# Kernel optimization log

Hardware: AMD Instinct MI355X
Metric: run time of the kernel (lower is better)

Reference implementation:

```python
import jax, jax.numpy as jnp
import numpy as np

BIG = 1e9
EPS_BETA = 1e-6
EPS_BN = 1e-5

N_NODES = 50000
N_EDGES = 800000
IN_DIM = 128
OUT_DIM = 128


def setup_inputs() -> dict:
    key = jax.random.key(0)
    ks = jax.random.split(key, 8)
    h = jax.random.normal(ks[0], (N_NODES, IN_DIM), dtype=jnp.float32)
    src = jax.random.randint(ks[1], (N_EDGES,), 0, N_NODES, dtype=jnp.int32)
    dst = jax.random.randint(ks[2], (N_EDGES,), 0, N_NODES, dtype=jnp.int32)
    sigma_GD = jax.random.uniform(ks[3], (N_EDGES,), dtype=jnp.float32)
    fc_w = jax.random.normal(ks[4], (IN_DIM, OUT_DIM), dtype=jnp.float32) / np.sqrt(IN_DIM)
    fc_b = jax.random.normal(ks[5], (OUT_DIM,), dtype=jnp.float32) * 0.01
    attn_w = jax.random.normal(ks[6], (2 * OUT_DIM, 1), dtype=jnp.float32) / np.sqrt(2 * OUT_DIM)
    attn_b = jax.random.normal(ks[7], (1,), dtype=jnp.float32) * 0.01
    bn_gamma = jnp.ones((OUT_DIM,), dtype=jnp.float32)
    bn_beta = jnp.zeros((OUT_DIM,), dtype=jnp.float32)
    return {"h": h, "src": src, "dst": dst, "sigma_GD": sigma_GD,
            "fc_w": fc_w, "fc_b": fc_b, "attn_w": attn_w, "attn_b": attn_b,
            "bn_gamma": bn_gamma, "bn_beta": bn_beta}


def reference(h, src, dst, sigma_GD, fc_w, fc_b, attn_w, attn_b, bn_gamma, bn_beta):
    n = h.shape[0]
    # node projection
    z = h @ fc_w + fc_b                                   # [N, D]
    z = jnp.where(jnp.isinf(z), BIG, z)
    # per-edge attention logits: concat(src,dst) @ W == src@W1 + dst@W2 (avoid concat materialization)
    d = z.shape[1]
    w_src, w_dst = attn_w[:d], attn_w[d:]
    z_src = z[src]                                        # [E, D]
    a = z_src @ w_src + z[dst] @ w_dst + attn_b           # [E, 1]
    a = jnp.where(jnp.isinf(a), BIG, a)
    e = jax.nn.leaky_relu(a, negative_slope=0.01)[:, 0]   # [E]
    # segment softmax over incoming edges (mailbox softmax)
    m = jax.ops.segment_max(e, dst, num_segments=n)       # [N]
    ex = jnp.exp(e - m[dst])
    denom = jax.ops.segment_sum(ex, dst, num_segments=n)  # [N]
    alpha = ex / denom[dst]                               # [E]
    # beta: sigma_GD normalized per destination node
    bsum = jax.ops.segment_sum(sigma_GD, dst, num_segments=n)
    beta = sigma_GD / (bsum[dst] + EPS_BETA)              # [E]
    # weighted scatter-sum of source features
    h_new = jax.ops.segment_sum((alpha * beta)[:, None] * z_src, dst, num_segments=n)  # [N, D]
    h_new = jnp.where(jnp.isinf(h_new), BIG, h_new)
    # BatchNorm1d (training-mode batch stats, biased variance, as torch does)
    mu = h_new.mean(axis=0)
    var = ((h_new - mu) ** 2).mean(axis=0)
    h_bn = (h_new - mu) * jax.lax.rsqrt(var + EPS_BN) * bn_gamma + bn_beta
    return jax.nn.elu(h_bn)
```

## Files before the change

### kernel.cpp

```cpp
#include <hip/hip_runtime.h>
#include <hip/hip_fp16.h>
#include <math.h>

#define N_NODES 50000
#define N_EDGES 800000
#define BIGV 1000000000.0f
#define NBLK_GEMM 3125
#define CHUNK 1024
#define NCHUNK 782
#define NBUCKET 782
#define NB4 784
#define NHALF 1564
#define BMAX 768
#define OVFSTRIDE 1024

typedef _Float16 half8 __attribute__((ext_vector_type(8)));
typedef float floatx4 __attribute__((ext_vector_type(4)));

__device__ __forceinline__ float clampinf(float x) { return isinf(x) ? BIGV : x; }

__device__ __forceinline__ void barrier_lgkm_only() {
    __builtin_amdgcn_sched_barrier(0);
    asm volatile("s_waitcnt lgkmcnt(0)" ::: "memory");
    __builtin_amdgcn_s_barrier();
    __builtin_amdgcn_sched_barrier(0);
}

__global__ __launch_bounds__(256) void k_prep(const float* __restrict__ W,
                                              __half* __restrict__ wt,
                                              float* __restrict__ bns,
                                              const int* __restrict__ dst,
                                              int* __restrict__ countsT)
{
    __shared__ int hist[NB4];
    const int t = threadIdx.x;
    const int idx = blockIdx.x * 256 + t;
    if (idx < 16384) {
        int n = idx >> 7, k = idx & 127;
        wt[idx] = __float2half(W[k * 128 + n]);
    }
    if (idx < 256) bns[idx] = 0.f;
    for (int i = t; i < NB4; i += 256) hist[i] = 0;
    __syncthreads();
    const int base = blockIdx.x * CHUNK;
    for (int i = t; i < CHUNK; i += 256) {
        int e = base + i;
        if (e < N_EDGES) atomicAdd(&hist[dst[e] >> 6], 1);
    }
    __syncthreads();
    for (int i = t; i < NB4; i += 256)
        countsT[i * NB4 + blockIdx.x] = hist[i];
}

__global__ __launch_bounds__(256) void k_off(const int* __restrict__ countsT,
                                             int* __restrict__ cursC,
                                             int* __restrict__ btot)
{
    const int wv = (blockIdx.x << 2) + (threadIdx.x >> 6);
    const int l = threadIdx.x & 63;
    if (wv >= NBUCKET) {
        if (l == 0 && wv < NB4) btot[wv] = 0;
        return;
    }
    const int* row = countsT + (size_t)wv * NB4;
    int carry = 0;
    #pragma unroll
    for (int p = 0; p < 13; ++p) {
        const int c = p * 64 + l;
        const int v = (c < NCHUNK) ? row[c] : 0;
        int x = v;
        #pragma unroll
        for (int o = 1; o < 64; o <<= 1) {
            int u = __shfl_up(x, o);
            if (l >= o) x += u;
        }
        if (c < NCHUNK) cursC[(size_t)c * NB4 + wv] = carry + x - v;
        carry += __shfl(x, 63);
    }
    if (l == 0) btot[wv] = carry;
}

__global__ __launch_bounds__(256) void k_gemm(
    const float* __restrict__ h, const __half* __restrict__ wt,
    const float* __restrict__ bias, const float* __restrict__ attn_w,
    __half* __restrict__ zh, float* __restrict__ sv, float* __restrict__ tv)
{
    __shared__ _Float16 hA[16][136];
    __shared__ float spart[4][16], tpart[4][16];

    const int tid = threadIdx.x;
    const int lane = tid & 63;
    const int wv = tid >> 6;
    const int l16 = lane & 15;
    const int oct = lane >> 4;
    const int n0 = wv << 5;
    const int node0 = blockIdx.x << 4;

    {
        const float4* h4 = (const float4*)(h + (size_t)node0 * 128);
        for (int i = tid; i < 512; i += 256) {
            int r = i >> 5, c4 = i & 31;
            float4 v = h4[i];
            union { __half2 h2[2]; uint2 u; } pk;
            pk.h2[0] = __floats2half2_rn(v.x, v.y);
            pk.h2[1] = __floats2half2_rn(v.z, v.w);
            *(uint2*)&hA[r][c4 << 2] = pk.u;
        }
    }

    half8 bfrag[4][2];
    #pragma unroll
    for (int kk = 0; kk < 4; ++kk)
        #pragma unroll
        for (int t = 0; t < 2; ++t)
            bfrag[kk][t] = *(const half8*)(wt + (size_t)(n0 + t * 16 + l16) * 128
                                              + kk * 32 + oct * 8);

    const float bv0 = bias[n0 + l16],         bv1 = bias[n0 + 16 + l16];
    const float ws0 = attn_w[n0 + l16],       ws1 = attn_w[n0 + 16 + l16];
    const float wd0 = attn_w[128 + n0 + l16], wd1 = attn_w[128 + n0 + 16 + l16];

    barrier_lgkm_only();

    floatx4 acc0 = {0.f, 0.f, 0.f, 0.f};
    floatx4 acc1 = {0.f, 0.f, 0.f, 0.f};
    #pragma unroll
    for (int kk = 0; kk < 4; ++kk) {
        half8 a = *(const half8*)&hA[l16][(kk << 5) + (oct << 3)];
        acc0 = __builtin_amdgcn_mfma_f32_16x16x32_f16(a, bfrag[kk][0], acc0, 0, 0, 0);
        acc1 = __builtin_amdgcn_mfma_f32_16x16x32_f16(a, bfrag[kk][1], acc1, 0, 0, 0);
    }

    float s_acc[4], t_acc[4];
    #pragma unroll
    for (int r = 0; r < 4; ++r) {
        float z0 = clampinf(acc0[r] + bv0);
        float z1 = clampinf(acc1[r] + bv1);
        const int row = (oct << 2) + r;
        zh[(size_t)(node0 + row) * 128 + n0 + l16]      = __float2half(z0);
        zh[(size_t)(node0 + row) * 128 + n0 + 16 + l16] = __float2half(z1);
        s_acc[r] = z0 * ws0 + z1 * ws1;
        t_acc[r] = z0 * wd0 + z1 * wd1;
    }
    #pragma unroll
    for (int r = 0; r < 4; ++r) {
        #pragma unroll
        for (int o = 1; o < 16; o <<= 1) {
            s_acc[r] += __shfl_xor(s_acc[r], o);
            t_acc[r] += __shfl_xor(t_acc[r], o);
        }
    }
    if (l16 == 0) {
        #pragma unroll
        for (int r = 0; r < 4; ++r) {
            spart[wv][(oct << 2) + r] = s_acc[r];
            tpart[wv][(oct << 2) + r] = t_acc[r];
        }
    }
    barrier_lgkm_only();
    if (tid < 16) {
        sv[node0 + tid] = spart[0][tid] + spart[1][tid] + spart[2][tid] + spart[3][tid];
        tv[node0 + tid] = tpart[0][tid] + tpart[1][tid] + tpart[2][tid] + tpart[3][tid];
    }
}

__global__ __launch_bounds__(256) void k_scat(
    const int* __restrict__ src, const int* __restrict__ dst,
    const float* __restrict__ sigma,
    const float* __restrict__ sv, const float* __restrict__ tv,
    const float* __restrict__ attn_b,
    const int* __restrict__ cursC, const int* __restrict__ btot,
    float4* __restrict__ tmp, int* __restrict__ bbase_g)
{
    __shared__ int cur[NB4];
    __shared__ int bb[NB4];
    __shared__ int tsc[256];
    const int t = threadIdx.x;
    const int self = blockIdx.x;

    for (int i = t; i < NB4; i += 256) cur[i] = cursC[(size_t)self * NB4 + i];

    uint4 bt = {0u, 0u, 0u, 0u};
    int tsum = 0;
    if (t < 196) {
        bt = ((const uint4*)btot)[t];
        tsum = (int)(bt.x + bt.y + bt.z + bt.w);
    }
    tsc[t] = tsum;
    __syncthreads();
    for (int off = 1; off < 256; off <<= 1) {
        int u = (t >= off) ? tsc[t - off] : 0;
        __syncthreads();
        tsc[t] += u;
        __syncthreads();
    }
    if (t < 196) {
        const int v0 = tsc[t] - tsum;
        bb[4*t+0] = v0;
        bb[4*t+1] = v0 + (int)bt.x;
        bb[4*t+2] = v0 + (int)bt.x + (int)bt.y;
        bb[4*t+3] = v0 + (int)bt.x + (int)bt.y + (int)bt.z;
    }
    __syncthreads();
    for (int i = t; i < NB4; i += 256) cur[i] += bb[i];
    if (self == 0)
        for (int i = t; i < NB4; i += 256) bbase_g[i] = bb[i];
    __syncthreads();

    const float ab = attn_b[0];
    const int base = self * CHUNK;
    for (int i = t; i < CHUNK; i += 256) {
        int e = base + i;
        if (e < N_EDGES) {
            int s = src[e];
            int d = dst[e];
            float a = sv[s] + tv[d] + ab;
            a = clampinf(a);
            float ev = a > 0.f ? a : 0.01f * a;
            int pos = atomicAdd(&cur[d >> 6], 1);
            float4 rec;
            rec.x = __int_as_float(s);
            rec.y = sigma[e];
            rec.z = ev;
            rec.w = __int_as_float(d);
            tmp[pos] = rec;
        }
    }
}

__global__ __launch_bounds__(512) void k_bagg(
    const float4* __restrict__ tmp, const int* __restrict__ bbase_g,
    const __half* __restrict__ zh, float4* __restrict__ ovf,
    float* __restrict__ out, float* __restrict__ partials)
{
    __shared__ float4 lrec[BMAX];
    __shared__ int hist[32];
    __shared__ int segs[33];
    __shared__ int cur[32];
    __shared__ float bnS[128], bnQ[128];
    const int t = threadIdx.x;
    const int b2 = blockIdx.x;
    const int b  = b2 >> 1;
    const int hf = b2 & 1;
    const int s0 = bbase_g[b];
    const int n  = bbase_g[b + 1] - s0;

    if (t < 32) hist[t] = 0;
    if (t < 128) { bnS[t] = 0.f; bnQ[t] = 0.f; }
    __syncthreads();
    const float* tw = (const float*)tmp;
    for (int i = t; i < n; i += 512) {
        int d = __float_as_int(tw[4 * (size_t)(s0 + i) + 3]);
        if (((d >> 5) & 1) == hf) atomicAdd(&hist[d & 31], 1);
    }
    __syncthreads();
    if (t < 32) {
        const int hv = hist[t];
        int x = hv;
        #pragma unroll
        for (int o = 1; o < 32; o <<= 1) {
            int u = __shfl_up(x, o);
            if (t >= o) x += u;
        }
        segs[t] = x - hv;
        cur[t]  = x - hv;
        if (t == 31) segs[32] = x;
    }
    __syncthreads();
    for (int i = t; i < n; i += 512) {
        float4 rec = tmp[s0 + i];
        int d = __float_as_int(rec.w);
        if (((d >> 5) & 1) == hf) {
            int pos = atomicAdd(&cur[d & 31], 1);
            if (pos < BMAX) lrec[pos] = rec;
            else            ovf[(size_t)b2 * OVFSTRIDE + (pos - BMAX)] = rec;
        }
    }
    __syncthreads();

    const int lane = t & 63;
    const int wv = t >> 6;
    const int grp = lane >> 4;
    const int l16 = lane & 15;
    float pS[8] = {0.f,0.f,0.f,0.f,0.f,0.f,0.f,0.f};
    float pQ[8] = {0.f,0.f,0.f,0.f,0.f,0.f,0.f,0.f};

    for (int j = wv; j < 32; j += 8) {
        const int node = (b << 6) + (hf << 5) + j;
        if (node >= N_NODES) continue;
        const int beg = segs[j];
        const int deg = segs[j + 1] - beg;
        float acc[8] = {0.f,0.f,0.f,0.f,0.f,0.f,0.f,0.f};

        if (deg > 0) {
            if (deg <= 64) {
                int sidx = 0; float sig = 0.f, e = -INFINITY;
                if (lane < deg) {
                    const int off = beg + lane;
                    float4 r = (off < BMAX) ? lrec[off]
                             : ovf[(size_t)b2 * OVFSTRIDE + (off - BMAX)];
                    sidx = __float_as_int(r.x); sig = r.y; e = r.z;
                }
                float m = e;
                for (int o = 32; o; o >>= 1) m = fmaxf(m, __shfl_xor(m, o));
                float p = (lane < deg) ? __expf(e - m) : 0.f;
                float dn = p, bs = sig;
                for (int o = 32; o; o >>= 1) {
                    dn += __shfl_xor(dn, o);
                    bs += __shfl_xor(bs, o);
                }
                const float coef = p * sig * (1.0f / dn) / (bs + 1e-6f);
                for (int c = 0; c < deg; c += 8) {
                    const int j0 = c + grp, j1 = c + 4 + grp;
                    const int js0 = (j0 < deg) ? j0 : 0;
                    const int js1 = (j1 < deg) ? j1 : 0;
                    float cf0 = __shfl(coef, js0); int sj0 = __shfl(sidx, js0);
                    float cf1 = __shfl(coef, js1); int sj1 = __shfl(sidx, js1);
                    uint4 raw0, raw1;
                    if (j0 < deg)
                        raw0 = *(const uint4*)(zh + ((size_t)sj0 << 7) + (l16 << 3));
                    if (j1 < deg)
                        raw1 = *(const uint4*)(zh + ((size_t)sj1 << 7) + (l16 << 3));
                    if (j0 < deg) {
                        const __half2* hp = (const __half2*)&raw0;
                        #pragma unroll
                        for (int k = 0; k < 4; ++k) {
                            float2 f = __half22float2(hp[k]);
                            acc[2*k]   = fmaf(cf0, f.x, acc[2*k]);
                            acc[2*k+1] = fmaf(cf0, f.y, acc[2*k+1]);
                        }
                    }
                    if (j1 < deg) {
                        const __half2* hp = (const __half2*)&raw1;
                        #pragma unroll
                        for (int k = 0; k < 4; ++k) {
                            float2 f = __half22float2(hp[k]);
                            acc[2*k]   = fmaf(cf1, f.x, acc[2*k]);
                            acc[2*k+1] = fmaf(cf1, f.y, acc[2*k+1]);
                        }
                    }
                }
            } else {
                float m = -INFINITY;
                for (int i = lane; i < deg; i += 64) {
                    const int off = beg + i;
                    float4 r = (off < BMAX) ? lrec[off]
                             : ovf[(size_t)b2 * OVFSTRIDE + (off - BMAX)];
                    m = fmaxf(m, r.z);
                }
                for (int o = 32; o; o >>= 1) m = fmaxf(m, __shfl_xor(m, o));
                float dn = 0.f, bs = 0.f;
                for (int i = lane; i < deg; i += 64) {
                    const int off = beg + i;
                    float4 r = (off < BMAX) ? lrec[off]
                             : ovf[(size_t)b2 * OVFSTRIDE + (off - BMAX)];
                    dn += __expf(r.z - m); bs += r.y;
                }
                for (int o = 32; o; o >>= 1) {
                    dn += __shfl_xor(dn, o);
                    bs += __shfl_xor(bs, o);
                }
                const float scale = (1.0f / dn) / (bs + 1e-6f);
                for (int c = 0; c < deg; c += 64) {
                    int i = c + lane;
                    int sidx = 0; float coef = 0.f;
                    if (i < deg) {
                        const int off = beg + i;
                        float4 r = (off < BMAX) ? lrec[off]
                                 : ovf[(size_t)b2 * OVFSTRIDE + (off - BMAX)];
                        sidx = __float_as_int(r.x);
                        coef = __expf(r.z - m) * r.y * scale;
                    }
                    const int cnt2 = min(64, deg - c);
                    for (int jj = 0; jj < cnt2; jj += 4) {
                        const int j4 = jj + grp;
                        const int js = (j4 < cnt2) ? j4 : 0;
                        float cf = __shfl(coef, js);
                        int sj = __shfl(sidx, js);
                        if (j4 < cnt2) {
                            uint4 raw = *(const uint4*)(zh + ((size_t)sj << 7) + (l16 << 3));
                            const __half2* hp = (const __half2*)&raw;
                            #pragma unroll
                            for (int k = 0; k < 4; ++k) {
                                float2 f = __half22float2(hp[k]);
                                acc[2*k]   = fmaf(cf, f.x, acc[2*k]);
                                acc[2*k+1] = fmaf(cf, f.y, acc[2*k+1]);
                            }
                        }
                    }
                }
            }
        }
        #pragma unroll
        for (int k = 0; k < 8; ++k) {
            acc[k] += __shfl_xor(acc[k], 16);
            acc[k] += __shfl_xor(acc[k], 32);
        }
        if (grp == 0) {
            float o[8];
            #pragma unroll
            for (int k = 0; k < 8; ++k) {
                o[k] = clampinf(acc[k]);
                pS[k] += o[k];
                pQ[k] += o[k] * o[k];
            }
            float4 o0, o1;
            o0.x = o[0]; o0.y = o[1]; o0.z = o[2]; o0.w = o[3];
            o1.x = o[4]; o1.y = o[5]; o1.z = o[6]; o1.w = o[7];
            float4* op = (float4*)(out + (size_t)node * 128 + (l16 << 3));
            op[0] = o0; op[1] = o1;
        }
    }
    if (grp == 0) {
        #pragma unroll
        for (int k = 0; k < 8; ++k) {
            atomicAdd(&bnS[(l16 << 3) + k], pS[k]);
            atomicAdd(&bnQ[(l16 << 3) + k], pQ[k]);
        }
    }
    __syncthreads();
    if (t < 128) {
        partials[(size_t)b2 * 256 + t]       = bnS[t];
        partials[(size_t)b2 * 256 + 128 + t] = bnQ[t];
    }
}

__global__ __launch_bounds__(256) void k_bnred(const float* __restrict__ partials,
                                               float* __restrict__ bns)
{
    const int t = threadIdx.x;
    const int r0 = blockIdx.x * 25;
    const int r1 = min(r0 + 25, NHALF);
    float s = 0.f;
    for (int r = r0; r < r1; ++r) s += partials[(size_t)r * 256 + t];
    atomicAdd(&bns[t], s);
}

__global__ __launch_bounds__(256) void k_bnapply(float* __restrict__ io,
                                                 const float* __restrict__ sums,
                                                 const float* __restrict__ gamma,
                                                 const float* __restrict__ beta)
{
    __shared__ float sc[128], sh[128];
    const int tid = threadIdx.x;
    if (tid < 128) {
        const float invn = 1.0f / (float)N_NODES;
        float mu = sums[tid] * invn;
        float var = fmaxf(sums[128 + tid] * invn - mu * mu, 0.f);
        float g = gamma[tid] * rsqrtf(var + 1e-5f);
        sc[tid] = g;
        sh[tid] = beta[tid] - mu * g;
    }
    __syncthreads();
    const size_t idx = (size_t)blockIdx.x * 256 + tid;
    const int f4 = ((int)idx & 31) << 2;
    float4 x = ((const float4*)io)[idx];
    float y0 = x.x * sc[f4 + 0] + sh[f4 + 0];
    float y1 = x.y * sc[f4 + 1] + sh[f4 + 1];
    float y2 = x.z * sc[f4 + 2] + sh[f4 + 2];
    float y3 = x.w * sc[f4 + 3] + sh[f4 + 3];
    float4 o;
    o.x = y0 > 0.f ? y0 : expm1f(y0);
    o.y = y1 > 0.f ? y1 : expm1f(y1);
    o.z = y2 > 0.f ? y2 : expm1f(y2);
    o.w = y3 > 0.f ? y3 : expm1f(y3);
    ((float4*)io)[idx] = o;
}

extern "C" void kernel_launch(void* const* d_in, const int* in_sizes, int n_in,
                              void* d_out, int out_size, void* d_ws, size_t ws_size,
                              hipStream_t stream)
{
    const float* h      = (const float*)d_in[0];
    const int*   src    = (const int*)  d_in[1];
    const int*   dst    = (const int*)  d_in[2];
    const float* sigma  = (const float*)d_in[3];
    const float* fc_w   = (const float*)d_in[4];
    const float* fc_b   = (const float*)d_in[5];
    const float* attn_w = (const float*)d_in[6];
    const float* attn_b = (const float*)d_in[7];
    const float* gamma  = (const float*)d_in[8];
    const float* beta   = (const float*)d_in[9];
    float* out = (float*)d_out;

    float4* tmp    = (float4*)d_ws;
    float4* ovf    = tmp + N_EDGES;
    __half* zh     = (__half*)(ovf + (size_t)NHALF * OVFSTRIDE);
    float*  sv     = (float*)(zh + (size_t)N_NODES * 128);
    float*  tv     = sv + N_NODES;
    float*  bns    = tv + N_NODES;
    float*  parts  = bns + 256;
    __half* wt     = (__half*)(parts + (size_t)NHALF * 256);
    int*    countsT= (int*)(wt + 16384);
    int*    cursC  = countsT + NB4 * NB4;
    int*    btot   = cursC + NB4 * NB4;
    int*    bbase  = btot + NB4;

    k_prep    <<<NCHUNK, 256, 0, stream>>>(fc_w, wt, bns, dst, countsT);
    k_off     <<<196, 256, 0, stream>>>(countsT, cursC, btot);
    k_gemm    <<<NBLK_GEMM, 256, 0, stream>>>(h, wt, fc_b, attn_w, zh, sv, tv);
    k_scat    <<<NCHUNK, 256, 0, stream>>>(src, dst, sigma, sv, tv, attn_b,
                                           cursC, btot, tmp, bbase);
    k_bagg    <<<NHALF, 512, 0, stream>>>(tmp, bbase, zh, ovf, out, parts);
    k_bnred   <<<64, 256, 0, stream>>>(parts, bns);
    k_bnapply <<<(N_NODES * 128) / (256 * 4), 256, 0, stream>>>(out, bns, gamma, beta);
}
```

Before: 232.2 us.

## Bucket edges by 32-node groups to remove duplicate half-bucket scanning

Result: no change. 235.9 us (+1.6%).

```diff
diff --git a/kernel.cpp b/kernel.cpp
--- a/kernel.cpp
+++ b/kernel.cpp
@@ -8,9 +8,9 @@
 #define NBLK_GEMM 3125
 #define CHUNK 1024
 #define NCHUNK 782
-#define NBUCKET 782
-#define NB4 784
-#define NHALF 1564
+#define NCH4 784
+#define NBUCKET 1563
+#define NBK4 1564
 #define BMAX 768
 #define OVFSTRIDE 1024
 
@@ -32,7 +32,7 @@
                                               const int* __restrict__ dst,
                                               int* __restrict__ countsT)
 {
-    __shared__ int hist[NB4];
+    __shared__ int hist[NBK4];
     const int t = threadIdx.x;
     const int idx = blockIdx.x * 256 + t;
     if (idx < 16384) {
@@ -40,16 +40,16 @@
         wt[idx] = __float2half(W[k * 128 + n]);
     }
     if (idx < 256) bns[idx] = 0.f;
-    for (int i = t; i < NB4; i += 256) hist[i] = 0;
+    for (int i = t; i < NBK4; i += 256) hist[i] = 0;
     __syncthreads();
     const int base = blockIdx.x * CHUNK;
     for (int i = t; i < CHUNK; i += 256) {
         int e = base + i;
-        if (e < N_EDGES) atomicAdd(&hist[dst[e] >> 6], 1);
-    }
-    __syncthreads();
-    for (int i = t; i < NB4; i += 256)
-        countsT[i * NB4 + blockIdx.x] = hist[i];
+        if (e < N_EDGES) atomicAdd(&hist[dst[e] >> 5], 1);
+    }
+    __syncthreads();
+    for (int i = t; i < NBK4; i += 256)
+        countsT[(size_t)i * NCH4 + blockIdx.x] = hist[i];
 }
 
 __global__ __launch_bounds__(256) void k_off(const int* __restrict__ countsT,
@@ -59,10 +59,10 @@
     const int wv = (blockIdx.x << 2) + (threadIdx.x >> 6);
     const int l = threadIdx.x & 63;
     if (wv >= NBUCKET) {
-        if (l == 0 && wv < NB4) btot[wv] = 0;
+        if (l == 0 && wv < NBK4) btot[wv] = 0;
         return;
     }
-    const int* row = countsT + (size_t)wv * NB4;
+    const int* row = countsT + (size_t)wv * NCH4;
     int carry = 0;
     #pragma unroll
     for (int p = 0; p < 13; ++p) {
@@ -74,7 +74,7 @@
             int u = __shfl_up(x, o);
             if (l >= o) x += u;
         }
-        if (c < NCHUNK) cursC[(size_t)c * NB4 + wv] = carry + x - v;
+        if (c < NCHUNK) cursC[(size_t)c * NBK4 + wv] = carry + x - v;
         carry += __shfl(x, 63);
     }
     if (l == 0) btot[wv] = carry;
@@ -164,7 +164,7 @@
     }
 }
 
-__global__ __launch_bounds__(256) void k_scat(
+__global__ __launch_bounds__(512) void k_scat(
     const int* __restrict__ src, const int* __restrict__ dst,
     const float* __restrict__ sigma,
     const float* __restrict__ sv, const float* __restrict__ tv,
@@ -172,29 +172,29 @@
     const int* __restrict__ cursC, const int* __restrict__ btot,
     float4* __restrict__ tmp, int* __restrict__ bbase_g)
 {
-    __shared__ int cur[NB4];
-    __shared__ int bb[NB4];
-    __shared__ int tsc[256];
+    __shared__ int cur[NBK4];
+    __shared__ int bb[NBK4];
+    __shared__ int tsc[512];
     const int t = threadIdx.x;
     const int self = blockIdx.x;
 
-    for (int i = t; i < NB4; i += 256) cur[i] = cursC[(size_t)self * NB4 + i];
+    for (int i = t; i < NBK4; i += 512) cur[i] = cursC[(size_t)self * NBK4 + i];
 
     uint4 bt = {0u, 0u, 0u, 0u};
     int tsum = 0;
-    if (t < 196) {
+    if (t < NBK4 / 4) {
         bt = ((const uint4*)btot)[t];
         tsum = (int)(bt.x + bt.y + bt.z + bt.w);
     }
     tsc[t] = tsum;
     __syncthreads();
-    for (int off = 1; off < 256; off <<= 1) {
+    for (int off = 1; off < 512; off <<= 1) {
         int u = (t >= off) ? tsc[t - off] : 0;
         __syncthreads();
         tsc[t] += u;
         __syncthreads();
     }
-    if (t < 196) {
+    if (t < NBK4 / 4) {
         const int v0 = tsc[t] - tsum;
         bb[4*t+0] = v0;
         bb[4*t+1] = v0 + (int)bt.x;
@@ -202,14 +202,14 @@
         bb[4*t+3] = v0 + (int)bt.x + (int)bt.y + (int)bt.z;
     }
     __syncthreads();
-    for (int i = t; i < NB4; i += 256) cur[i] += bb[i];
+    for (int i = t; i < NBK4; i += 512) cur[i] += bb[i];
     if (self == 0)
-        for (int i = t; i < NB4; i += 256) bbase_g[i] = bb[i];
+        for (int i = t; i < NBK4; i += 512) bbase_g[i] = bb[i];
     __syncthreads();
 
     const float ab = attn_b[0];
     const int base = self * CHUNK;
-    for (int i = t; i < CHUNK; i += 256) {
+    for (int i = t; i < CHUNK; i += 512) {
         int e = base + i;
         if (e < N_EDGES) {
             int s = src[e];
@@ -217,7 +217,7 @@
             float a = sv[s] + tv[d] + ab;
             a = clampinf(a);
             float ev = a > 0.f ? a : 0.01f * a;
-            int pos = atomicAdd(&cur[d >> 6], 1);
+            int pos = atomicAdd(&cur[d >> 5], 1);
             float4 rec;
             rec.x = __int_as_float(s);
             rec.y = sigma[e];
@@ -239,9 +239,7 @@
     __shared__ int cur[32];
     __shared__ float bnS[128], bnQ[128];
     const int t = threadIdx.x;
-    const int b2 = blockIdx.x;
-    const int b  = b2 >> 1;
-    const int hf = b2 & 1;
+    const int b = blockIdx.x;
     const int s0 = bbase_g[b];
     const int n  = bbase_g[b + 1] - s0;
 
@@ -251,7 +249,7 @@
     const float* tw = (const float*)tmp;
     for (int i = t; i < n; i += 512) {
         int d = __float_as_int(tw[4 * (size_t)(s0 + i) + 3]);
-        if (((d >> 5) & 1) == hf) atomicAdd(&hist[d & 31], 1);
+        atomicAdd(&hist[d & 31], 1);
     }
     __syncthreads();
     if (t < 32) {
@@ -270,11 +268,9 @@
     for (int i = t; i < n; i += 512) {
         float4 rec = tmp[s0 + i];
         int d = __float_as_int(rec.w);
-        if (((d >> 5) & 1) == hf) {
-            int pos = atomicAdd(&cur[d & 31], 1);
-            if (pos < BMAX) lrec[pos] = rec;
-            else            ovf[(size_t)b2 * OVFSTRIDE + (pos - BMAX)] = rec;
-        }
+        int pos = atomicAdd(&cur[d & 31], 1);
+        if (pos < BMAX) lrec[pos] = rec;
+        else            ovf[(size_t)b * OVFSTRIDE + (pos - BMAX)] = rec;
     }
     __syncthreads();
 
@@ -286,7 +282,7 @@
     float pQ[8] = {0.f,0.f,0.f,0.f,0.f,0.f,0.f,0.f};
 
     for (int j = wv; j < 32; j += 8) {
-        const int node = (b << 6) + (hf << 5) + j;
+        const int node = (b << 5) + j;
         if (node >= N_NODES) continue;
         const int beg = segs[j];
         const int deg = segs[j + 1] - beg;
@@ -298,7 +294,7 @@
                 if (lane < deg) {
                     const int off = beg + lane;
                     float4 r = (off < BMAX) ? lrec[off]
-                             : ovf[(size_t)b2 * OVFSTRIDE + (off - BMAX)];
+                             : ovf[(size_t)b * OVFSTRIDE + (off - BMAX)];
                     sidx = __float_as_int(r.x); sig = r.y; e = r.z;
                 }
                 float m = e;
@@ -345,7 +341,7 @@
                 for (int i = lane; i < deg; i += 64) {
                     const int off = beg + i;
                     float4 r = (off < BMAX) ? lrec[off]
-                             : ovf[(size_t)b2 * OVFSTRIDE + (off - BMAX)];
+                             : ovf[(size_t)b * OVFSTRIDE + (off - BMAX)];
                     m = fmaxf(m, r.z);
                 }
                 for (int o = 32; o; o >>= 1) m = fmaxf(m, __shfl_xor(m, o));
@@ -353,7 +349,7 @@
                 for (int i = lane; i < deg; i += 64) {
                     const int off = beg + i;
                     float4 r = (off < BMAX) ? lrec[off]
-                             : ovf[(size_t)b2 * OVFSTRIDE + (off - BMAX)];
+                             : ovf[(size_t)b * OVFSTRIDE + (off - BMAX)];
                     dn += __expf(r.z - m); bs += r.y;
                 }
                 for (int o = 32; o; o >>= 1) {
@@ -367,7 +363,7 @@
                     if (i < deg) {
                         const int off = beg + i;
                         float4 r = (off < BMAX) ? lrec[off]
-                                 : ovf[(size_t)b2 * OVFSTRIDE + (off - BMAX)];
+                                 : ovf[(size_t)b * OVFSTRIDE + (off - BMAX)];
                         sidx = __float_as_int(r.x);
                         coef = __expf(r.z - m) * r.y * scale;
                     }
@@ -420,8 +416,8 @@
     }
     __syncthreads();
     if (t < 128) {
-        partials[(size_t)b2 * 256 + t]       = bnS[t];
-        partials[(size_t)b2 * 256 + 128 + t] = bnQ[t];
+        partials[(size_t)b * 256 + t]       = bnS[t];
+        partials[(size_t)b * 256 + 128 + t] = bnQ[t];
     }
 }
 
@@ -430,7 +426,7 @@
 {
     const int t = threadIdx.x;
     const int r0 = blockIdx.x * 25;
-    const int r1 = min(r0 + 25, NHALF);
+    const int r1 = min(r0 + 25, NBUCKET);
     float s = 0.f;
     for (int r = r0; r < r1; ++r) s += partials[(size_t)r * 256 + t];
     atomicAdd(&bns[t], s);
@@ -485,23 +481,23 @@
 
     float4* tmp    = (float4*)d_ws;
     float4* ovf    = tmp + N_EDGES;
-    __half* zh     = (__half*)(ovf + (size_t)NHALF * OVFSTRIDE);
+    __half* zh     = (__half*)(ovf + (size_t)NBK4 * OVFSTRIDE);
     float*  sv     = (float*)(zh + (size_t)N_NODES * 128);
     float*  tv     = sv + N_NODES;
     float*  bns    = tv + N_NODES;
     float*  parts  = bns + 256;
-    __half* wt     = (__half*)(parts + (size_t)NHALF * 256);
+    __half* wt     = (__half*)(parts + (size_t)NBK4 * 256);
     int*    countsT= (int*)(wt + 16384);
-    int*    cursC  = countsT + NB4 * NB4;
-    int*    btot   = cursC + NB4 * NB4;
-    int*    bbase  = btot + NB4;
+    int*    cursC  = countsT + (size_t)NBK4 * NCH4;
+    int*    btot   = cursC + (size_t)NCH4 * NBK4;
+    int*    bbase  = btot + NBK4;
 
     k_prep    <<<NCHUNK, 256, 0, stream>>>(fc_w, wt, bns, dst, countsT);
-    k_off     <<<196, 256, 0, stream>>>(countsT, cursC, btot);
+    k_off     <<<NBK4 / 4, 256, 0, stream>>>(countsT, cursC, btot);
     k_gemm    <<<NBLK_GEMM, 256, 0, stream>>>(h, wt, fc_b, attn_w, zh, sv, tv);
-    k_scat    <<<NCHUNK, 256, 0, stream>>>(src, dst, sigma, sv, tv, attn_b,
+    k_scat    <<<NCHUNK, 512, 0, stream>>>(src, dst, sigma, sv, tv, attn_b,
                                            cursC, btot, tmp, bbase);
-    k_bagg    <<<NHALF, 512, 0, stream>>>(tmp, bbase, zh, ovf, out, parts);
+    k_bagg    <<<NBUCKET, 512, 0, stream>>>(tmp, bbase, zh, ovf, out, parts);
     k_bnred   <<<64, 256, 0, stream>>>(parts, bns);
     k_bnapply <<<(N_NODES * 128) / (256 * 4), 256, 0, stream>>>(out, bns, gamma, beta);
 }
```
